# Kernel optimization log

Hardware: AMD Instinct MI355X
Metric: run time of the kernel (lower is better)

The kernel has to match this reference:

```python
import jax, jax.numpy as jnp
import numpy as np

B, T, C, H, L, V = 2, 1024, 768, 12, 12, 50257
D = C // H  # head size = 64
EPS = 1e-5


def _layer_norm(x, w, b):
    m = x.mean(-1, keepdims=True)
    v = x.var(-1, keepdims=True)
    return (x - m) * jax.lax.rsqrt(v + EPS) * w + b


def setup_inputs() -> dict:
    key = jax.random.key(0)
    ks = jax.random.split(key, 8)
    std = 0.02
    res_std = 0.02 * (2 * L) ** -0.5  # NANOGPT_SCALE_INIT
    rn = lambda k, shape, s: jax.random.normal(k, shape, jnp.float32) * s
    return dict(
        idx=jax.random.randint(ks[0], (B, T), 0, V),
        wte=rn(ks[1], (V, C), std),
        wpe=rn(ks[2], (T, C), std),
        ln1_w=jnp.ones((L, C), jnp.float32), ln1_b=jnp.zeros((L, C), jnp.float32),
        qkv_w=rn(ks[3], (L, C, 3 * C), std), qkv_b=jnp.zeros((L, 3 * C), jnp.float32),
        proj_w=rn(ks[4], (L, C, C), res_std), proj_b=jnp.zeros((L, C), jnp.float32),
        ln2_w=jnp.ones((L, C), jnp.float32), ln2_b=jnp.zeros((L, C), jnp.float32),
        fc_w=rn(ks[5], (L, C, 4 * C), std), fc_b=jnp.zeros((L, 4 * C), jnp.float32),
        fco_w=rn(ks[6], (L, 4 * C, C), res_std), fco_b=jnp.zeros((L, C), jnp.float32),
        lnf_w=jnp.ones((C,), jnp.float32), lnf_b=jnp.zeros((C,), jnp.float32),
    )


def reference(idx, wte, wpe, ln1_w, ln1_b, qkv_w, qkv_b, proj_w, proj_b,
              ln2_w, ln2_b, fc_w, fc_b, fco_w, fco_b, lnf_w, lnf_b):
    x = wte[idx] + wpe[:T]  # [B, T, C] tok + pos emb
    mask = jnp.tril(jnp.ones((T, T), bool))  # causal
    scale = 1.0 / np.sqrt(D).astype(np.float32)

    def block(x, p):
        l1w, l1b, qw, qb, pw, pb, l2w, l2b, fw, fb, fow, fob = p
        h = _layer_norm(x, l1w, l1b)
        qkv = h @ qw + qb  # [B, T, 3C]
        q, k, v = jnp.split(qkv, 3, axis=-1)
        q = q.reshape(B, T, H, D)
        k = k.reshape(B, T, H, D)
        v = v.reshape(B, T, H, D)
        att = jnp.einsum('bqhd,bkhd->bhqk', q, k) * scale
        att = jnp.where(mask, att, -jnp.inf)
        att = jax.nn.softmax(att, axis=-1)
        y = jnp.einsum('bhqk,bkhd->bqhd', att, v).reshape(B, T, C)
        x = x + y @ pw + pb
        h2 = _layer_norm(x, l2w, l2b)
        x = x + jax.nn.gelu(h2 @ fw + fb, approximate=True) @ fow + fob
        return x, None

    x, _ = jax.lax.scan(block, x, (ln1_w, ln1_b, qkv_w, qkv_b, proj_w, proj_b,
                                   ln2_w, ln2_b, fc_w, fc_b, fco_w, fco_b))
    x = _layer_norm(x, lnf_w, lnf_b)
    logits = x @ wte.T  # tied lm_head
    return logits
```

## Files before the change

### kernel.cpp

```cpp
#include <hip/hip_runtime.h>
#include <cmath>
#include <cstdint>

#define T_SEQ 1024
#define NH 12
#define NL 12
#define NV 50257
#define CD 768
#define M_ROWS 2048

typedef __bf16 bf16_t;
typedef __bf16 bf16x8 __attribute__((ext_vector_type(8)));
typedef float f32x4 __attribute__((ext_vector_type(4)));

__device__ __forceinline__ void gload16(const bf16_t* g, bf16_t* l) {
  __builtin_amdgcn_global_load_lds(
      (const __attribute__((address_space(1))) void*)g,
      (__attribute__((address_space(3))) void*)l, 16, 0, 0);
}

__global__ __launch_bounds__(256) void embed_k(const int* __restrict__ idx,
    const float* __restrict__ wte, const float* __restrict__ wpe,
    float* __restrict__ x) {
  int m = blockIdx.x;
  int t = m & (T_SEQ - 1);
  int tok = idx[m];
  const float* a = wte + (size_t)tok * CD;
  const float* p = wpe + (size_t)t * CD;
  float* xr = x + (size_t)m * CD;
  int c = threadIdx.x;
  xr[c]       = a[c]       + p[c];
  xr[c + 256] = a[c + 256] + p[c + 256];
  xr[c + 512] = a[c + 512] + p[c + 512];
}

__global__ __launch_bounds__(256) void cvt_k(const float* __restrict__ in,
    bf16_t* __restrict__ out, int n4) {
  int i = blockIdx.x * 256 + threadIdx.x;
  if (i < n4) {
    float4 v = ((const float4*)in)[i];
    bf16_t* o = out + (size_t)i * 4;
    o[0] = (bf16_t)v.x; o[1] = (bf16_t)v.y;
    o[2] = (bf16_t)v.z; o[3] = (bf16_t)v.w;
  }
}

__global__ __launch_bounds__(256) void transcvt_k(const float* __restrict__ W,
    bf16_t* __restrict__ WT, int K, int N) {
  __shared__ float tl[32][33];
  int k0 = blockIdx.y * 32, n0 = blockIdx.x * 32;
  int j = threadIdx.x & 31, i0 = threadIdx.x >> 5;
  #pragma unroll
  for (int i = i0; i < 32; i += 8) tl[i][j] = W[(size_t)(k0 + i) * N + n0 + j];
  __syncthreads();
  #pragma unroll
  for (int i = i0; i < 32; i += 8)
    WT[(size_t)(n0 + i) * K + k0 + j] = (bf16_t)tl[j][i];
}

__global__ __launch_bounds__(256) void ln_k(const float* __restrict__ x,
    const float* __restrict__ w, const float* __restrict__ bi,
    bf16_t* __restrict__ out) {
  int row = blockIdx.x;
  const float* xr = x + (size_t)row * CD;
  int t = threadIdx.x;
  float v0 = xr[t], v1 = xr[t + 256], v2 = xr[t + 512];
  float s = v0 + v1 + v2;
  float ss = v0 * v0 + v1 * v1 + v2 * v2;
  #pragma unroll
  for (int o = 1; o < 64; o <<= 1) { s += __shfl_xor(s, o); ss += __shfl_xor(ss, o); }
  __shared__ float sh[8];
  int wid = t >> 6, lane = t & 63;
  if (lane == 0) { sh[wid] = s; sh[4 + wid] = ss; }
  __syncthreads();
  s  = sh[0] + sh[1] + sh[2] + sh[3];
  ss = sh[4] + sh[5] + sh[6] + sh[7];
  float mean = s * (1.f / CD);
  float var  = ss * (1.f / CD) - mean * mean;
  float rs = rsqrtf(var + 1e-5f);
  bf16_t* orow = out + (size_t)row * CD;
  orow[t]       = (bf16_t)((v0 - mean) * rs * w[t]       + bi[t]);
  orow[t + 256] = (bf16_t)((v1 - mean) * rs * w[t + 256] + bi[t + 256]);
  orow[t + 512] = (bf16_t)((v2 - mean) * rs * w[t + 512] + bi[t + 512]);
}

template <int BM, int BN, int EPI, bool SWAP, bool XSWZ>
__global__ __launch_bounds__(256) void gemm_bt(
    const bf16_t* __restrict__ A,
    const bf16_t* __restrict__ BT,
    const float* __restrict__ bias,
    const float* __restrict__ resid,
    void* __restrict__ out_p,
    int Mdim, int Ndim, int Kdim) {
  constexpr int MR = BM / 32, NR = BN / 32;
  __shared__ __align__(1024) bf16_t As[BM * 64];
  __shared__ __align__(1024) bf16_t Bs[BN * 64];
  const int t = threadIdx.x;
  const int wid = t >> 6, lane = t & 63;
  const int wm = wid >> 1, wn = wid & 1;
  int bx = blockIdx.x, by = blockIdx.y;
  if (XSWZ) {
    int gx = gridDim.x;
    int lin = by * gx + bx;
    int cpx = (gx * gridDim.y) >> 3;
    int swz = (lin & 7) * cpx + (lin >> 3);
    bx = swz % gx; by = swz / gx;
  }
  const int m0 = (SWAP ? bx : by) * BM;
  const int n0 = (SWAP ? by : bx) * BN;
  const int l15 = lane & 15, lhi = lane >> 4;

  const int srow = lane >> 3;
  const int schk = lane & 7;

  f32x4 acc[MR][NR] = {};

  for (int kt = 0; kt < Kdim; kt += 64) {
    #pragma unroll
    for (int i = 0; i < BM / 32; ++i) {
      int rbase = wid * (BM / 4) + i * 8;
      int r = rbase + srow;
      int c = schk ^ (r & 7);
      gload16(A + (size_t)(m0 + r) * Kdim + kt + c * 8, As + rbase * 64);
    }
    #pragma unroll
    for (int i = 0; i < BN / 32; ++i) {
      int rbase = wid * (BN / 4) + i * 8;
      int r = rbase + srow;
      int nr = n0 + r; if (nr >= Ndim) nr = Ndim - 1;
      int c = schk ^ (r & 7);
      gload16(BT + (size_t)nr * Kdim + kt + c * 8, Bs + rbase * 64);
    }
    __syncthreads();

    #pragma unroll
    for (int ks = 0; ks < 2; ++ks) {
      bf16x8 af[MR], bfr[NR];
      #pragma unroll
      for (int mm = 0; mm < MR; ++mm) {
        int ra = wm * (BM / 2) + mm * 16 + l15;
        af[mm] = *(const bf16x8*)&As[ra * 64 + (((ks * 4 + lhi) ^ (ra & 7)) * 8)];
      }
      #pragma unroll
      for (int nn = 0; nn < NR; ++nn) {
        int rb = wn * (BN / 2) + nn * 16 + l15;
        bfr[nn] = *(const bf16x8*)&Bs[rb * 64 + (((ks * 4 + lhi) ^ (rb & 7)) * 8)];
      }
      #pragma unroll
      for (int mm = 0; mm < MR; ++mm)
        #pragma unroll
        for (int nn = 0; nn < NR; ++nn)
          acc[mm][nn] = __builtin_amdgcn_mfma_f32_16x16x32_bf16(af[mm], bfr[nn], acc[mm][nn], 0, 0, 0);
    }
    __syncthreads();
  }

  bf16_t* ob = (bf16_t*)out_p;
  float*  of = (float*)out_p;
  const int row0 = m0 + wm * (BM / 2);
  const int col0 = n0 + wn * (BN / 2);
  #pragma unroll
  for (int mm = 0; mm < MR; ++mm) {
    #pragma unroll
    for (int nn = 0; nn < NR; ++nn) {
      int col = col0 + nn * 16 + l15;
      if (col >= Ndim) continue;
      float bv = (EPI != 3) ? bias[col] : 0.f;
      #pragma unroll
      for (int r = 0; r < 4; ++r) {
        int row = row0 + mm * 16 + lhi * 4 + r;
        float v = acc[mm][nn][r] + bv;
        size_t o = (size_t)row * Ndim + col;
        if (EPI == 0) {
          ob[o] = (bf16_t)v;
        } else if (EPI == 1) {
          float u = v + 0.044715f * v * v * v;
          v = 0.5f * v * (1.f + tanhf(0.79788456080286536f * u));
          ob[o] = (bf16_t)v;
        } else if (EPI == 2) {
          of[o] = resid[o] + v;
        } else {
          of[o] = v;
        }
      }
    }
  }
}

__global__ __launch_bounds__(256) void vtrans_k(const bf16_t* __restrict__ qkv,
                                                bf16_t* __restrict__ VT) {
  __shared__ __align__(16) bf16_t tl[64 * 72];
  const int bh = blockIdx.y;
  const int t0 = blockIdx.x * 64;
  const int b = bh / NH, h = bh % NH;
  const int tid = threadIdx.x;
  const int row = tid >> 2;
  const int seg = (tid & 3) * 16;

  const bf16_t* src = qkv + (size_t)(b * T_SEQ + t0 + row) * (3 * CD) + 2 * CD + h * 64 + seg;
  bf16x8 v0 = *(const bf16x8*)src;
  bf16x8 v1 = *(const bf16x8*)(src + 8);
  #pragma unroll
  for (int j = 0; j < 8; ++j) tl[(seg + j) * 72 + row] = v0[j];
  #pragma unroll
  for (int j = 0; j < 8; ++j) tl[(seg + 8 + j) * 72 + row] = v1[j];
  __syncthreads();

  bf16_t* dst = VT + ((size_t)bh * 64 + row) * T_SEQ + t0 + seg;
  *(bf16x8*)dst       = *(const bf16x8*)&tl[row * 72 + seg];
  *(bf16x8*)(dst + 8) = *(const bf16x8*)&tl[row * 72 + seg + 8];
}

__global__ __launch_bounds__(64) void attn_k(const bf16_t* __restrict__ qkv,
                                             const bf16_t* __restrict__ VT,
                                             bf16_t* __restrict__ y) {
  __shared__ __align__(16) bf16_t Ps[16 * 40];
  const int lane = threadIdx.x;
  const int gw = blockIdx.x;
  const int qi = gw & 63;
  const int bh = gw >> 6;
  const int h = bh % NH, b = bh / NH;
  const bf16_t* Qbase = qkv + (size_t)b * T_SEQ * (3 * CD) + h * 64;
  const bf16_t* Kbase = Qbase + CD;
  const bf16_t* Vt = VT + (size_t)bh * 64 * T_SEQ;

  const int l15 = lane & 15, lhi = lane >> 4;
  const int q0 = qi * 16;

  bf16x8 aq[2];
  #pragma unroll
  for (int c = 0; c < 2; ++c)
    aq[c] = *(const bf16x8*)(Qbase + (size_t)(q0 + l15) * (3 * CD) + c * 32 + lhi * 8);

  f32x4 acc[4] = {};
  float m_[4], l_[4];
  #pragma unroll
  for (int r = 0; r < 4; ++r) { m_[r] = -INFINITY; l_[r] = 0.f; }

  const int qrow = q0 + lhi * 4;
  const int nt = (q0 + 47) / 32;
  for (int kt = 0; kt < nt; ++kt) {
    const int k0 = kt * 32;
    f32x4 s[2] = {};
    #pragma unroll
    for (int c = 0; c < 2; ++c) {
      #pragma unroll
      for (int kc = 0; kc < 2; ++kc) {
        bf16x8 bk = *(const bf16x8*)(Kbase + (size_t)(k0 + kc * 16 + l15) * (3 * CD) + c * 32 + lhi * 8);
        s[kc] = __builtin_amdgcn_mfma_f32_16x16x32_bf16(aq[c], bk, s[kc], 0, 0, 0);
      }
    }
    float mx[4];
    #pragma unroll
    for (int r = 0; r < 4; ++r) mx[r] = -INFINITY;
    #pragma unroll
    for (int kc = 0; kc < 2; ++kc) {
      const int kcol = k0 + kc * 16 + l15;
      #pragma unroll
      for (int r = 0; r < 4; ++r) {
        float sv = (kcol <= qrow + r) ? s[kc][r] * 0.125f : -INFINITY;
        s[kc][r] = sv;
        mx[r] = fmaxf(mx[r], sv);
      }
    }
    #pragma unroll
    for (int r = 0; r < 4; ++r) {
      mx[r] = fmaxf(mx[r], __shfl_xor(mx[r], 1));
      mx[r] = fmaxf(mx[r], __shfl_xor(mx[r], 2));
      mx[r] = fmaxf(mx[r], __shfl_xor(mx[r], 4));
      mx[r] = fmaxf(mx[r], __shfl_xor(mx[r], 8));
    }
    float al[4], rs[4];
    #pragma unroll
    for (int r = 0; r < 4; ++r) {
      float mn = fmaxf(m_[r], mx[r]);
      al[r] = __expf(m_[r] - mn);
      m_[r] = mn;
      float p0 = __expf(s[0][r] - mn);
      float p1 = __expf(s[1][r] - mn);
      s[0][r] = p0; s[1][r] = p1;
      rs[r] = p0 + p1;
    }
    #pragma unroll
    for (int r = 0; r < 4; ++r) {
      rs[r] += __shfl_xor(rs[r], 1);
      rs[r] += __shfl_xor(rs[r], 2);
      rs[r] += __shfl_xor(rs[r], 4);
      rs[r] += __shfl_xor(rs[r], 8);
      l_[r] = l_[r] * al[r] + rs[r];
    }
    #pragma unroll
    for (int dt = 0; dt < 4; ++dt)
      #pragma unroll
      for (int r = 0; r < 4; ++r) acc[dt][r] *= al[r];
    #pragma unroll
    for (int kc = 0; kc < 2; ++kc)
      #pragma unroll
      for (int r = 0; r < 4; ++r)
        Ps[(lhi * 4 + r) * 40 + kc * 16 + l15] = (bf16_t)s[kc][r];
    bf16x8 pa = *(const bf16x8*)&Ps[l15 * 40 + lhi * 8];
    #pragma unroll
    for (int dt = 0; dt < 4; ++dt) {
      bf16x8 bv = *(const bf16x8*)(Vt + (size_t)(dt * 16 + l15) * T_SEQ + k0 + lhi * 8);
      acc[dt] = __builtin_amdgcn_mfma_f32_16x16x32_bf16(pa, bv, acc[dt], 0, 0, 0);
    }
  }
  #pragma unroll
  for (int dt = 0; dt < 4; ++dt)
    #pragma unroll
    for (int r = 0; r < 4; ++r)
      y[(size_t)(b * T_SEQ + q0 + lhi * 4 + r) * CD + h * 64 + dt * 16 + l15] =
          (bf16_t)(acc[dt][r] / l_[r]);
}

extern "C" void kernel_launch(void* const* d_in, const int* in_sizes, int n_in,
                              void* d_out, int out_size, void* d_ws, size_t ws_size,
                              hipStream_t stream) {
  const int*   idx   = (const int*)d_in[0];
  const float* wte   = (const float*)d_in[1];
  const float* wpe   = (const float*)d_in[2];
  const float* ln1w  = (const float*)d_in[3];
  const float* ln1b  = (const float*)d_in[4];
  const float* qkvw  = (const float*)d_in[5];
  const float* qkvb  = (const float*)d_in[6];
  const float* projw = (const float*)d_in[7];
  const float* projb = (const float*)d_in[8];
  const float* ln2w  = (const float*)d_in[9];
  const float* ln2b  = (const float*)d_in[10];
  const float* fcw   = (const float*)d_in[11];
  const float* fcb   = (const float*)d_in[12];
  const float* fcow  = (const float*)d_in[13];
  const float* fcob  = (const float*)d_in[14];
  const float* lnfw  = (const float*)d_in[15];
  const float* lnfb  = (const float*)d_in[16];
  float* out = (float*)d_out;

  char* w = (char*)d_ws;
  auto alloc = [&](size_t bytes) {
    char* p = w; w += (bytes + 255) & ~(size_t)255; return p;
  };
  float*  x    = (float*)alloc((size_t)M_ROWS * CD * 4);
  float*  x2   = (float*)alloc((size_t)M_ROWS * CD * 4);
  bf16_t* hb   = (bf16_t*)alloc((size_t)M_ROWS * CD * 2);
  bf16_t* qkvB = (bf16_t*)alloc((size_t)M_ROWS * 3 * CD * 2);
  bf16_t* yb   = (bf16_t*)alloc((size_t)M_ROWS * CD * 2);
  bf16_t* fca  = (bf16_t*)alloc((size_t)M_ROWS * 4 * CD * 2);
  bf16_t* VT   = (bf16_t*)alloc((size_t)2 * NH * 64 * T_SEQ * 2);
  bf16_t* wqT  = (bf16_t*)alloc((size_t)3 * CD * CD * 2);
  bf16_t* wpT  = (bf16_t*)alloc((size_t)CD * CD * 2);
  bf16_t* wfT  = (bf16_t*)alloc((size_t)4 * CD * CD * 2);
  bf16_t* woT  = (bf16_t*)alloc((size_t)CD * 4 * CD * 2);
  bf16_t* wteB = (bf16_t*)alloc((size_t)NV * CD * 2);

  embed_k<<<M_ROWS, 256, 0, stream>>>(idx, wte, wpe, x);
  {
    int n4 = NV * CD / 4;
    cvt_k<<<(n4 + 255) / 256, 256, 0, stream>>>(wte, wteB, n4);
  }

  for (int l = 0; l < NL; ++l) {
    transcvt_k<<<dim3(3 * CD / 32, CD / 32), 256, 0, stream>>>(qkvw  + (size_t)l * CD * 3 * CD, wqT, CD, 3 * CD);
    transcvt_k<<<dim3(CD / 32, CD / 32),     256, 0, stream>>>(projw + (size_t)l * CD * CD,     wpT, CD, CD);
    transcvt_k<<<dim3(4 * CD / 32, CD / 32), 256, 0, stream>>>(fcw   + (size_t)l * CD * 4 * CD, wfT, CD, 4 * CD);
    transcvt_k<<<dim3(CD / 32, 4 * CD / 32), 256, 0, stream>>>(fcow  + (size_t)l * 4 * CD * CD, woT, 4 * CD, CD);

    ln_k<<<M_ROWS, 256, 0, stream>>>(x, ln1w + l * CD, ln1b + l * CD, hb);
    gemm_bt<128, 128, 0, false, false><<<dim3(3 * CD / 128, M_ROWS / 128), 256, 0, stream>>>(
        hb, wqT, qkvb + l * 3 * CD, nullptr, qkvB, M_ROWS, 3 * CD, CD);
    vtrans_k<<<dim3(T_SEQ / 64, 2 * NH), 256, 0, stream>>>(qkvB, VT);
    attn_k<<<2 * NH * 64, 64, 0, stream>>>(qkvB, VT, yb);
    gemm_bt<64, 64, 2, false, false><<<dim3(CD / 64, M_ROWS / 64), 256, 0, stream>>>(
        yb, wpT, projb + l * CD, x, x2, M_ROWS, CD, CD);
    ln_k<<<M_ROWS, 256, 0, stream>>>(x2, ln2w + l * CD, ln2b + l * CD, hb);
    gemm_bt<128, 128, 1, false, false><<<dim3(4 * CD / 128, M_ROWS / 128), 256, 0, stream>>>(
        hb, wfT, fcb + l * 4 * CD, nullptr, fca, M_ROWS, 4 * CD, CD);
    gemm_bt<64, 64, 2, false, false><<<dim3(CD / 64, M_ROWS / 64), 256, 0, stream>>>(
        fca, woT, fcob + l * CD, x2, x, M_ROWS, CD, 4 * CD);
  }

  ln_k<<<M_ROWS, 256, 0, stream>>>(x, lnfw, lnfb, hb);
  gemm_bt<128, 128, 3, true, true><<<dim3(M_ROWS / 128, (NV + 127) / 128), 256, 0, stream>>>(
      hb, wteB, nullptr, nullptr, out, M_ROWS, NV, CD);
}
```

Before: 2.407 ms.

## Double-buffer GEMM LDS tiles and batch per-layer weight transposes into single launches

The GEMM k-loop now uses two LDS buffers with a 32-wide k slice, issuing the async global-to-LDS load for the next slice before computing on the current one. This removes one barrier per iteration and overlaps loads with MFMA work, at the cost of twice as many iterations with less compute per sync. Separately, when the workspace is large enough, all twelve layers' weights are transposed and converted in four batched launches using blockIdx.z, instead of four launches per layer. This cuts launch count but uses much more workspace memory.

```diff
diff --git a/kernel.cpp b/kernel.cpp
--- a/kernel.cpp
+++ b/kernel.cpp
@@ -45,8 +45,10 @@
   }
 }
 
-__global__ __launch_bounds__(256) void transcvt_k(const float* __restrict__ W,
-    bf16_t* __restrict__ WT, int K, int N) {
+__global__ __launch_bounds__(256) void transcvt_k(const float* __restrict__ W0,
+    bf16_t* __restrict__ WT0, int K, int N) {
+  const float* W = W0 + (size_t)blockIdx.z * K * N;
+  bf16_t* WT = WT0 + (size_t)blockIdx.z * N * K;
   __shared__ float tl[32][33];
   int k0 = blockIdx.y * 32, n0 = blockIdx.x * 32;
   int j = threadIdx.x & 31, i0 = threadIdx.x >> 5;
@@ -93,8 +95,8 @@
     void* __restrict__ out_p,
     int Mdim, int Ndim, int Kdim) {
   constexpr int MR = BM / 32, NR = BN / 32;
-  __shared__ __align__(1024) bf16_t As[BM * 64];
-  __shared__ __align__(1024) bf16_t Bs[BN * 64];
+  __shared__ __align__(1024) bf16_t As[2][BM * 32];
+  __shared__ __align__(1024) bf16_t Bs[2][BN * 32];
   const int t = threadIdx.x;
   const int wid = t >> 6, lane = t & 63;
   const int wm = wid >> 1, wn = wid & 1;
@@ -110,49 +112,54 @@
   const int n0 = (SWAP ? by : bx) * BN;
   const int l15 = lane & 15, lhi = lane >> 4;
 
-  const int srow = lane >> 3;
-  const int schk = lane & 7;
-
-  f32x4 acc[MR][NR] = {};
-
-  for (int kt = 0; kt < Kdim; kt += 64) {
-    #pragma unroll
-    for (int i = 0; i < BM / 32; ++i) {
-      int rbase = wid * (BM / 4) + i * 8;
+  const int srow = lane >> 2;
+  const int schk = lane & 3;
+
+  auto stage = [&](int buf, int kt) {
+    #pragma unroll
+    for (int i = 0; i < BM / 64; ++i) {
+      int rbase = wid * (BM / 4) + i * 16;
       int r = rbase + srow;
-      int c = schk ^ (r & 7);
-      gload16(A + (size_t)(m0 + r) * Kdim + kt + c * 8, As + rbase * 64);
-    }
-    #pragma unroll
-    for (int i = 0; i < BN / 32; ++i) {
-      int rbase = wid * (BN / 4) + i * 8;
+      int c = schk ^ ((r >> 1) & 3);
+      gload16(A + (size_t)(m0 + r) * Kdim + kt + c * 8, &As[buf][rbase * 32]);
+    }
+    #pragma unroll
+    for (int i = 0; i < BN / 64; ++i) {
+      int rbase = wid * (BN / 4) + i * 16;
       int r = rbase + srow;
       int nr = n0 + r; if (nr >= Ndim) nr = Ndim - 1;
-      int c = schk ^ (r & 7);
-      gload16(BT + (size_t)nr * Kdim + kt + c * 8, Bs + rbase * 64);
-    }
+      int c = schk ^ ((r >> 1) & 3);
+      gload16(BT + (size_t)nr * Kdim + kt + c * 8, &Bs[buf][rbase * 32]);
+    }
+  };
+
+  f32x4 acc[MR][NR] = {};
+
+  stage(0, 0);
+  __syncthreads();
+  int cur = 0;
+  for (int kt = 0; kt < Kdim; kt += 32) {
+    if (kt + 32 < Kdim) stage(cur ^ 1, kt + 32);
+
+    bf16x8 af[MR], bfr[NR];
+    #pragma unroll
+    for (int mm = 0; mm < MR; ++mm) {
+      int ra = wm * (BM / 2) + mm * 16 + l15;
+      af[mm] = *(const bf16x8*)&As[cur][ra * 32 + ((lhi ^ (ra >> 1)) & 3) * 8];
+    }
+    #pragma unroll
+    for (int nn = 0; nn < NR; ++nn) {
+      int rb = wn * (BN / 2) + nn * 16 + l15;
+      bfr[nn] = *(const bf16x8*)&Bs[cur][rb * 32 + ((lhi ^ (rb >> 1)) & 3) * 8];
+    }
+    #pragma unroll
+    for (int mm = 0; mm < MR; ++mm)
+      #pragma unroll
+      for (int nn = 0; nn < NR; ++nn)
+        acc[mm][nn] = __builtin_amdgcn_mfma_f32_16x16x32_bf16(af[mm], bfr[nn], acc[mm][nn], 0, 0, 0);
+
     __syncthreads();
-
-    #pragma unroll
-    for (int ks = 0; ks < 2; ++ks) {
-      bf16x8 af[MR], bfr[NR];
-      #pragma unroll
-      for (int mm = 0; mm < MR; ++mm) {
-        int ra = wm * (BM / 2) + mm * 16 + l15;
-        af[mm] = *(const bf16x8*)&As[ra * 64 + (((ks * 4 + lhi) ^ (ra & 7)) * 8)];
-      }
-      #pragma unroll
-      for (int nn = 0; nn < NR; ++nn) {
-        int rb = wn * (BN / 2) + nn * 16 + l15;
-        bfr[nn] = *(const bf16x8*)&Bs[rb * 64 + (((ks * 4 + lhi) ^ (rb & 7)) * 8)];
-      }
-      #pragma unroll
-      for (int mm = 0; mm < MR; ++mm)
-        #pragma unroll
-        for (int nn = 0; nn < NR; ++nn)
-          acc[mm][nn] = __builtin_amdgcn_mfma_f32_16x16x32_bf16(af[mm], bfr[nn], acc[mm][nn], 0, 0, 0);
-    }
-    __syncthreads();
+    cur ^= 1;
   }
 
   bf16_t* ob = (bf16_t*)out_p;
@@ -346,23 +353,43 @@
   bf16_t* yb   = (bf16_t*)alloc((size_t)M_ROWS * CD * 2);
   bf16_t* fca  = (bf16_t*)alloc((size_t)M_ROWS * 4 * CD * 2);
   bf16_t* VT   = (bf16_t*)alloc((size_t)2 * NH * 64 * T_SEQ * 2);
-  bf16_t* wqT  = (bf16_t*)alloc((size_t)3 * CD * CD * 2);
-  bf16_t* wpT  = (bf16_t*)alloc((size_t)CD * CD * 2);
-  bf16_t* wfT  = (bf16_t*)alloc((size_t)4 * CD * CD * 2);
-  bf16_t* woT  = (bf16_t*)alloc((size_t)CD * 4 * CD * 2);
   bf16_t* wteB = (bf16_t*)alloc((size_t)NV * CD * 2);
+  bf16_t* wqT_s = (bf16_t*)alloc((size_t)3 * CD * CD * 2);
+  bf16_t* wpT_s = (bf16_t*)alloc((size_t)CD * CD * 2);
+  bf16_t* wfT_s = (bf16_t*)alloc((size_t)4 * CD * CD * 2);
+  bf16_t* woT_s = (bf16_t*)alloc((size_t)CD * 4 * CD * 2);
+  const size_t qkvSz = (size_t)3 * CD * CD, prSz = (size_t)CD * CD;
+  const size_t fcSz  = (size_t)4 * CD * CD, foSz = (size_t)CD * 4 * CD;
+  bf16_t* wqT_b = (bf16_t*)alloc(NL * qkvSz * 2);
+  bf16_t* wpT_b = (bf16_t*)alloc(NL * prSz * 2);
+  bf16_t* wfT_b = (bf16_t*)alloc(NL * fcSz * 2);
+  bf16_t* woT_b = (bf16_t*)alloc(NL * foSz * 2);
+  const bool big = (size_t)(w - (char*)d_ws) <= ws_size;
 
   embed_k<<<M_ROWS, 256, 0, stream>>>(idx, wte, wpe, x);
   {
     int n4 = NV * CD / 4;
     cvt_k<<<(n4 + 255) / 256, 256, 0, stream>>>(wte, wteB, n4);
   }
+  if (big) {
+    transcvt_k<<<dim3(3 * CD / 32, CD / 32, NL), 256, 0, stream>>>(qkvw,  wqT_b, CD, 3 * CD);
+    transcvt_k<<<dim3(CD / 32, CD / 32, NL),     256, 0, stream>>>(projw, wpT_b, CD, CD);
+    transcvt_k<<<dim3(4 * CD / 32, CD / 32, NL), 256, 0, stream>>>(fcw,   wfT_b, CD, 4 * CD);
+    transcvt_k<<<dim3(CD / 32, 4 * CD / 32, NL), 256, 0, stream>>>(fcow,  woT_b, 4 * CD, CD);
+  }
 
   for (int l = 0; l < NL; ++l) {
-    transcvt_k<<<dim3(3 * CD / 32, CD / 32), 256, 0, stream>>>(qkvw  + (size_t)l * CD * 3 * CD, wqT, CD, 3 * CD);
-    transcvt_k<<<dim3(CD / 32, CD / 32),     256, 0, stream>>>(projw + (size_t)l * CD * CD,     wpT, CD, CD);
-    transcvt_k<<<dim3(4 * CD / 32, CD / 32), 256, 0, stream>>>(fcw   + (size_t)l * CD * 4 * CD, wfT, CD, 4 * CD);
-    transcvt_k<<<dim3(CD / 32, 4 * CD / 32), 256, 0, stream>>>(fcow  + (size_t)l * 4 * CD * CD, woT, 4 * CD, CD);
+    bf16_t *wqT, *wpT, *wfT, *woT;
+    if (big) {
+      wqT = wqT_b + (size_t)l * qkvSz; wpT = wpT_b + (size_t)l * prSz;
+      wfT = wfT_b + (size_t)l * fcSz;  woT = woT_b + (size_t)l * foSz;
+    } else {
+      wqT = wqT_s; wpT = wpT_s; wfT = wfT_s; woT = woT_s;
+      transcvt_k<<<dim3(3 * CD / 32, CD / 32, 1), 256, 0, stream>>>(qkvw  + (size_t)l * CD * 3 * CD, wqT, CD, 3 * CD);
+      transcvt_k<<<dim3(CD / 32, CD / 32, 1),     256, 0, stream>>>(projw + (size_t)l * CD * CD,     wpT, CD, CD);
+      transcvt_k<<<dim3(4 * CD / 32, CD / 32, 1), 256, 0, stream>>>(fcw   + (size_t)l * CD * 4 * CD, wfT, CD, 4 * CD);
+      transcvt_k<<<dim3(CD / 32, 4 * CD / 32, 1), 256, 0, stream>>>(fcow  + (size_t)l * 4 * CD * CD, woT, 4 * CD, CD);
+    }
 
     ln_k<<<M_ROWS, 256, 0, stream>>>(x, ln1w + l * CD, ln1b + l * CD, hb);
     gemm_bt<128, 128, 0, false, false><<<dim3(3 * CD / 128, M_ROWS / 128), 256, 0, stream>>>(
```

Result: slower. 2.517 ms (+4.5%).
